# Performance work log

Measured on AMD Instinct MI355X. Metric: run time of the kernel, lower is better.

Reference implementation:

```python
import jax, jax.numpy as jnp
import numpy as np

B, N, D = 2, 2048, 2048
H, HKV, HD = 16, 4, 128  # n_heads, n_kv_heads, head_dim
G = H // HKV             # GQA group size


def setup_inputs() -> dict:
    key = jax.random.key(0)
    ks = jax.random.split(key, 5)
    x = jax.random.normal(ks[0], (B, N, D), jnp.float32)
    # rotary angles: standard 10000-base frequencies, half head_dim
    inv_freq = 1.0 / (10000.0 ** (jnp.arange(HD // 2, dtype=jnp.float32) / (HD // 2)))
    ang = jnp.arange(N, dtype=jnp.float32)[:, None] * inv_freq[None, :]  # [N, HD/2]
    cos = jnp.cos(ang)[None, :, None, :]  # [1, N, 1, HD/2]
    sin = jnp.sin(ang)[None, :, None, :]
    attn_mask = jnp.ones((B, N), jnp.float32)
    s = 0.02
    Wq = jax.random.normal(ks[1], (D, H * HD), jnp.float32) * s
    Wkv = jax.random.normal(ks[2], (D, 2 * HKV * HD), jnp.float32) * s
    Wo = jax.random.normal(ks[3], (H * HD, D), jnp.float32) * s
    bo = jnp.zeros((D,), jnp.float32)
    return {"x": x, "cos": cos, "sin": sin, "attn_mask": attn_mask,
            "Wq": Wq, "Wkv": Wkv, "Wo": Wo, "bo": bo}


def _rope(t, cos, sin):
    # t: [b, n, h, d]; rotate-half style split at d//2
    d2 = t.shape[-1] // 2
    t1, t2 = t[..., :d2], t[..., d2:]
    return jnp.concatenate([t1 * cos + t2 * sin, t2 * cos - t1 * sin], axis=-1)


def reference(x, cos, sin, attn_mask, Wq, Wkv, Wo, bo):
    b, n, _ = x.shape
    q = (x @ Wq).reshape(b, n, H, HD)
    kv = x @ Wkv
    k, v = jnp.split(kv, 2, axis=-1)
    k = k.reshape(b, n, HKV, HD)
    v = v.reshape(b, n, HKV, HD)
    q = _rope(q, cos, sin)
    k = _rope(k, cos, sin)
    # b n h d -> b h n d; group q heads: head H_idx maps to kv head H_idx % HKV
    # (einops '(r h)' repeat pattern => q reshaped as [b, G, HKV, n, d])
    q = q.transpose(0, 2, 1, 3).reshape(b, G, HKV, n, HD)
    k = k.transpose(0, 2, 1, 3)  # [b, HKV, n, d]
    v = v.transpose(0, 2, 1, 3)
    scale = HD ** -0.5
    attn = jnp.einsum('bghnd,bhmd->bghnm', q, k) * scale
    bias = (1.0 - attn_mask) * -1e9  # [b, n_keys]
    attn = attn + bias[:, None, None, None, :]
    attn = jax.nn.softmax(attn, axis=-1)
    out = jnp.einsum('bghnm,bhmd->bghnd', attn, v)
    # b (g h) n d -> b n (g h d)
    out = out.transpose(0, 3, 1, 2, 4).reshape(b, n, H * HD)
    return out @ Wo + bo
```

## Files before the change

### kernel.cpp

```cpp
#include <hip/hip_runtime.h>
#include <hip/hip_bf16.h>
#include <cstddef>

#define NB    2
#define NSEQ  2048
#define DMODEL 2048
#define NH    16
#define NKV   4
#define HDIM  128

typedef __attribute__((ext_vector_type(8))) short short8;
typedef __attribute__((ext_vector_type(4))) short short4v;
typedef __attribute__((ext_vector_type(4))) float floatx4;
typedef const __attribute__((address_space(1))) void* gptr_t;
typedef __attribute__((address_space(3))) void* lptr_t;

#if __has_builtin(__builtin_amdgcn_exp2f)
#define EXP2F(x) __builtin_amdgcn_exp2f(x)
#else
#define EXP2F(x) __expf((x) * 0.6931471805599453f)
#endif

__device__ inline unsigned short f2bf(float f) {
    unsigned int u = __float_as_uint(f);
    u += 0x7fffu + ((u >> 16) & 1u);
    return (unsigned short)(u >> 16);
}

__device__ inline floatx4 fzero4() {
    floatx4 v; v[0] = 0.f; v[1] = 0.f; v[2] = 0.f; v[3] = 0.f; return v;
}

__global__ void cast_f32_bf16(const float* __restrict__ in,
                              unsigned short* __restrict__ out, int n4) {
    int i = blockIdx.x * blockDim.x + threadIdx.x;
    if (i >= n4) return;
    float4 v = ((const float4*)in)[i];
    ushort4 o;
    o.x = f2bf(v.x); o.y = f2bf(v.y); o.z = f2bf(v.z); o.w = f2bf(v.w);
    ((ushort4*)out)[i] = o;
}

__global__ void transpose_cast(const float* __restrict__ W,
                               unsigned short* __restrict__ Wt, int K, int N) {
    __shared__ float tile[32][33];
    int tx = threadIdx.x, ty = threadIdx.y;
    int n0 = blockIdx.x * 32, k0 = blockIdx.y * 32;
#pragma unroll
    for (int i = 0; i < 4; i++)
        tile[ty + i * 8][tx] = W[(size_t)(k0 + ty + i * 8) * N + n0 + tx];
    __syncthreads();
#pragma unroll
    for (int i = 0; i < 4; i++)
        Wt[(size_t)(n0 + ty + i * 8) * K + k0 + tx] = f2bf(tile[tx][ty + i * 8]);
}

__global__ __launch_bounds__(256, 2) void gemm_bt(
    const unsigned short* __restrict__ A,
    const unsigned short* __restrict__ Bt,
    float* __restrict__ C,
    const float* __restrict__ bias,
    int M, int N, int K) {
    __shared__ __align__(16) unsigned short As[128 * 32];
    __shared__ __align__(16) unsigned short Bs[128 * 32];
    const int t = threadIdx.x;
    const int m0 = blockIdx.y * 128, n0 = blockIdx.x * 128;
    const int lane = t & 63, wave = t >> 6;
    const int ln = lane & 15, quad = lane >> 4;
    const int wm = (wave >> 1) * 64, wn = (wave & 1) * 64;
    floatx4 acc[4][4];
#pragma unroll
    for (int r = 0; r < 4; r++)
#pragma unroll
        for (int c = 0; c < 4; c++) acc[r][c] = fzero4();

    const int r0 = t >> 2, c0 = (t & 3) * 8;
    const int r1 = (t + 256) >> 2, c1 = ((t + 256) & 3) * 8;

    for (int kt = 0; kt < K; kt += 32) {
        const unsigned short* ga0 = A + (size_t)(m0 + r0) * K + kt + c0;
        const unsigned short* ga1 = A + (size_t)(m0 + r1) * K + kt + c1;
        const unsigned short* gb0 = Bt + (size_t)(n0 + r0) * K + kt + c0;
        const unsigned short* gb1 = Bt + (size_t)(n0 + r1) * K + kt + c1;
        __builtin_amdgcn_global_load_lds((gptr_t)ga0, (lptr_t)(As + t * 8), 16, 0, 0);
        __builtin_amdgcn_global_load_lds((gptr_t)ga1, (lptr_t)(As + (t + 256) * 8), 16, 0, 0);
        __builtin_amdgcn_global_load_lds((gptr_t)gb0, (lptr_t)(Bs + t * 8), 16, 0, 0);
        __builtin_amdgcn_global_load_lds((gptr_t)gb1, (lptr_t)(Bs + (t + 256) * 8), 16, 0, 0);
        __syncthreads();
        short8 af[4], bfr[4];
#pragma unroll
        for (int r = 0; r < 4; r++)
            af[r] = *(const short8*)(As + (wm + r * 16 + ln) * 32 + quad * 8);
#pragma unroll
        for (int c = 0; c < 4; c++)
            bfr[c] = *(const short8*)(Bs + (wn + c * 16 + ln) * 32 + quad * 8);
#pragma unroll
        for (int r = 0; r < 4; r++)
#pragma unroll
            for (int c = 0; c < 4; c++)
                acc[r][c] = __builtin_amdgcn_mfma_f32_16x16x32_bf16(af[r], bfr[c], acc[r][c], 0, 0, 0);
        __syncthreads();
    }
#pragma unroll
    for (int r = 0; r < 4; r++) {
        int mb = m0 + wm + r * 16 + quad * 4;
#pragma unroll
        for (int c = 0; c < 4; c++) {
            int col = n0 + wn + c * 16 + ln;
            float bv = bias ? bias[col] : 0.f;
#pragma unroll
            for (int g = 0; g < 4; g++)
                C[(size_t)(mb + g) * N + col] = acc[r][c][g] + bv;
        }
    }
}

__global__ void rope_q_k(const float* __restrict__ qkv, const float* __restrict__ cosb,
                         const float* __restrict__ sinb, unsigned short* __restrict__ Qb) {
    int idx = blockIdx.x * blockDim.x + threadIdx.x;
    int j = idx & 63;
    int h = (idx >> 6) & 15;
    int n = (idx >> 10) & 2047;
    int b = idx >> 21;
    const float scale = (float)(0.08838834764831845 * 1.4426950408889634);
    size_t row = (size_t)(b * NSEQ + n) * 3072;
    float t1 = qkv[row + h * 128 + j];
    float t2 = qkv[row + h * 128 + j + 64];
    float c = cosb[n * 64 + j], s = sinb[n * 64 + j];
    size_t orow = ((size_t)(b * NH + h) * NSEQ + n) * 128;
    Qb[orow + j]      = f2bf((t1 * c + t2 * s) * scale);
    Qb[orow + j + 64] = f2bf((t2 * c - t1 * s) * scale);
}

__global__ void rope_kv_k(const float* __restrict__ qkv, const float* __restrict__ cosb,
                          const float* __restrict__ sinb, unsigned short* __restrict__ Kb,
                          unsigned short* __restrict__ Vt) {
    int idx = blockIdx.x * blockDim.x + threadIdx.x;
    int j = idx & 63;
    int hk = (idx >> 6) & 3;
    int n = (idx >> 8) & 2047;
    int b = idx >> 19;
    size_t row = (size_t)(b * NSEQ + n) * 3072;
    float t1 = qkv[row + 2048 + hk * 128 + j];
    float t2 = qkv[row + 2048 + hk * 128 + j + 64];
    float c = cosb[n * 64 + j], s = sinb[n * 64 + j];
    size_t orow = ((size_t)(b * NKV + hk) * NSEQ + n) * 128;
    Kb[orow + j]      = f2bf(t1 * c + t2 * s);
    Kb[orow + j + 64] = f2bf(t2 * c - t1 * s);
    float v1 = qkv[row + 2560 + hk * 128 + j];
    float v2 = qkv[row + 2560 + hk * 128 + j + 64];
    int r = n & 63;
    int rp = ((r >> 5) << 5) | (((r >> 2) & 3) << 3) | (((r >> 4) & 1) << 2) | (r & 3);
    int np = (n & ~63) | rp;
    size_t vbase = (size_t)(b * NKV + hk) * 128 * NSEQ;
    Vt[vbase + (size_t)j * NSEQ + np]        = f2bf(v1);
    Vt[vbase + (size_t)(j + 64) * NSEQ + np] = f2bf(v2);
}

__global__ __launch_bounds__(256, 2) void attn_k(
    const unsigned short* __restrict__ Qb,
    const unsigned short* __restrict__ Kb,
    const unsigned short* __restrict__ Vt,
    const float* __restrict__ mask,
    unsigned short* __restrict__ Ab) {
    __shared__ __align__(16) unsigned short Ks[2 * 64 * 128];
    __shared__ __align__(16) unsigned short Vs[2 * 128 * 64];
    const int t = threadIdx.x, wave = t >> 6, lane = t & 63;
    const int ln = lane & 15, quad = lane >> 4;
    const int y = blockIdx.y, b = y >> 4, h = y & 15, kv = h & 3;
    const int q0 = blockIdx.x * 128;

    const unsigned short* Kbase = Kb + (size_t)(b * NKV + kv) * NSEQ * 128;
    const unsigned short* Vbase = Vt + (size_t)(b * NKV + kv) * 128 * NSEQ;
    const float* mbase = mask + b * NSEQ;

    const unsigned short* Qp =
        Qb + ((size_t)(b * NH + h) * NSEQ + q0 + wave * 32 + ln) * 128;
    short8 qf[2][4];
#pragma unroll
    for (int rt = 0; rt < 2; rt++)
#pragma unroll
        for (int kc = 0; kc < 4; kc++)
            qf[rt][kc] = *(const short8*)(Qp + rt * 16 * 128 + kc * 32 + quad * 8);

    floatx4 Oacc[2][8];
#pragma unroll
    for (int rt = 0; rt < 2; rt++)
#pragma unroll
        for (int d = 0; d < 8; d++) Oacc[rt][d] = fzero4();
    floatx4 Lacc[2];
    Lacc[0] = fzero4(); Lacc[1] = fzero4();

    short8 ones8;
#pragma unroll
    for (int i = 0; i < 8; i++) ones8[i] = (short)0x3F80;

    {
#pragma unroll
        for (int i = 0; i < 4; i++) {
            int c = i * 256 + t, r = c >> 4, c8 = c & 15;
            __builtin_amdgcn_global_load_lds(
                (gptr_t)(Kbase + (size_t)r * 128 + ((c8 ^ (r & 7)) * 8)),
                (lptr_t)(Ks + c * 8), 16, 0, 0);
        }
#pragma unroll
        for (int i = 0; i < 4; i++) {
            int c = i * 256 + t, dr = c >> 3, c8 = c & 7;
            __builtin_amdgcn_global_load_lds(
                (gptr_t)(Vbase + (size_t)dr * NSEQ + ((c8 ^ (dr & 7)) * 8)),
                (lptr_t)(Vs + c * 8), 16, 0, 0);
        }
    }
    __syncthreads();

    for (int it = 0; it < NSEQ / 64; ++it) {
        const int kt = it * 64, cb = it & 1;
        const int ktn = (kt + 64) & (NSEQ - 1);
        unsigned short* Kn = Ks + (cb ^ 1) * 8192;
        unsigned short* Vn = Vs + (cb ^ 1) * 8192;
#pragma unroll
        for (int i = 0; i < 4; i++) {
            int c = i * 256 + t, r = c >> 4, c8 = c & 15;
            __builtin_amdgcn_global_load_lds(
                (gptr_t)(Kbase + (size_t)(ktn + r) * 128 + ((c8 ^ (r & 7)) * 8)),
                (lptr_t)(Kn + c * 8), 16, 0, 0);
        }
#pragma unroll
        for (int i = 0; i < 4; i++) {
            int c = i * 256 + t, dr = c >> 3, c8 = c & 7;
            __builtin_amdgcn_global_load_lds(
                (gptr_t)(Vbase + (size_t)dr * NSEQ + ktn + ((c8 ^ (dr & 7)) * 8)),
                (lptr_t)(Vn + c * 8), 16, 0, 0);
        }

        floatx4 biasv[4];
#pragma unroll
        for (int nj = 0; nj < 4; nj++) {
            float4 mb = *(const float4*)(mbase + kt + nj * 16 + quad * 4);
            biasv[nj][0] = (1.f - mb.x) * -1.4426950408889634e9f;
            biasv[nj][1] = (1.f - mb.y) * -1.4426950408889634e9f;
            biasv[nj][2] = (1.f - mb.z) * -1.4426950408889634e9f;
            biasv[nj][3] = (1.f - mb.w) * -1.4426950408889634e9f;
        }

        const unsigned short* Kc = Ks + cb * 8192;
        const unsigned short* Vc = Vs + cb * 8192;

        floatx4 sacc[2][4];
#pragma unroll
        for (int rt = 0; rt < 2; rt++)
#pragma unroll
            for (int nj = 0; nj < 4; nj++) sacc[rt][nj] = fzero4();
#pragma unroll
        for (int kc = 0; kc < 4; kc++) {
            short8 kfv[4];
#pragma unroll
            for (int nj = 0; nj < 4; nj++)
                kfv[nj] = *(const short8*)(
                    Kc + (nj * 16 + ln) * 128 + (((kc * 4 + quad) ^ (ln & 7)) * 8));
#pragma unroll
            for (int rt = 0; rt < 2; rt++)
#pragma unroll
                for (int nj = 0; nj < 4; nj++)
                    sacc[rt][nj] = __builtin_amdgcn_mfma_f32_16x16x32_bf16(
                        kfv[nj], qf[rt][kc], sacc[rt][nj], 0, 0, 0);
        }

        short8 pf[2][2];
#pragma unroll
        for (int rt = 0; rt < 2; rt++)
#pragma unroll
            for (int p = 0; p < 2; p++)
#pragma unroll
                for (int e = 0; e < 2; e++) {
                    int nj = 2 * p + e;
#pragma unroll
                    for (int g = 0; g < 4; g++) {
                        float v = EXP2F(sacc[rt][nj][g] + biasv[nj][g]);
                        pf[rt][p][e * 4 + g] = (short)f2bf(v);
                    }
                }

#pragma unroll
        for (int rt = 0; rt < 2; rt++)
#pragma unroll
            for (int p = 0; p < 2; p++)
                Lacc[rt] = __builtin_amdgcn_mfma_f32_16x16x32_bf16(
                    ones8, pf[rt][p], Lacc[rt], 0, 0, 0);

#pragma unroll
        for (int dt = 0; dt < 8; dt++) {
            short8 vf[2];
#pragma unroll
            for (int p = 0; p < 2; p++)
                vf[p] = *(const short8*)(
                    Vc + (dt * 16 + ln) * 64 + (((p * 4 + quad) ^ (ln & 7)) * 8));
#pragma unroll
            for (int rt = 0; rt < 2; rt++) {
                floatx4 o = Oacc[rt][dt];
                o = __builtin_amdgcn_mfma_f32_16x16x32_bf16(vf[0], pf[rt][0], o, 0, 0, 0);
                o = __builtin_amdgcn_mfma_f32_16x16x32_bf16(vf[1], pf[rt][1], o, 0, 0, 0);
                Oacc[rt][dt] = o;
            }
        }
        __syncthreads();
    }

#pragma unroll
    for (int rt = 0; rt < 2; rt++) {
        float inv = 1.f / Lacc[rt][0];
        int row = q0 + wave * 32 + rt * 16 + ln;
        unsigned short* outp = Ab + (size_t)(b * NSEQ + row) * 2048 + h * 128;
#pragma unroll
        for (int dt = 0; dt < 8; dt++) {
            short4v o4;
#pragma unroll
            for (int g = 0; g < 4; g++) o4[g] = (short)f2bf(Oacc[rt][dt][g] * inv);
            *(short4v*)(outp + dt * 16 + quad * 4) = o4;
        }
    }
}

extern "C" void kernel_launch(void* const* d_in, const int* in_sizes, int n_in,
                              void* d_out, int out_size, void* d_ws, size_t ws_size,
                              hipStream_t stream) {
    const float* x    = (const float*)d_in[0];
    const float* cosb = (const float*)d_in[1];
    const float* sinb = (const float*)d_in[2];
    const float* mask = (const float*)d_in[3];
    const float* Wq   = (const float*)d_in[4];
    const float* Wkv  = (const float*)d_in[5];
    const float* Wo   = (const float*)d_in[6];
    const float* bo   = (const float*)d_in[7];
    float* out = (float*)d_out;

    char* ws = (char*)d_ws;
    unsigned short* xb  = (unsigned short*)ws; ws += (size_t)4096 * 2048 * 2;
    unsigned short* W1T = (unsigned short*)ws; ws += (size_t)3072 * 2048 * 2;
    unsigned short* WoT = (unsigned short*)ws; ws += (size_t)2048 * 2048 * 2;
    unsigned short* Qb  = (unsigned short*)ws; ws += (size_t)2 * 16 * 2048 * 128 * 2;
    unsigned short* Kb  = (unsigned short*)ws; ws += (size_t)2 * 4 * 2048 * 128 * 2;
    unsigned short* Vt  = (unsigned short*)ws; ws += (size_t)2 * 4 * 2048 * 128 * 2;
    float* qkv = (float*)ws;                   ws += (size_t)4096 * 3072 * 4;
    unsigned short* Ab = (unsigned short*)qkv;

    cast_f32_bf16<<<8192, 256, 0, stream>>>(x, xb, 2097152);
    dim3 tb(32, 8);
    transpose_cast<<<dim3(64, 64), tb, 0, stream>>>(Wq, W1T, 2048, 2048);
    transpose_cast<<<dim3(32, 64), tb, 0, stream>>>(Wkv, W1T + (size_t)2048 * 2048, 2048, 1024);
    transpose_cast<<<dim3(64, 64), tb, 0, stream>>>(Wo, WoT, 2048, 2048);
    gemm_bt<<<dim3(24, 32), 256, 0, stream>>>(xb, W1T, qkv, nullptr, 4096, 3072, 2048);
    rope_q_k<<<16384, 256, 0, stream>>>(qkv, cosb, sinb, Qb);
    rope_kv_k<<<4096, 256, 0, stream>>>(qkv, cosb, sinb, Kb, Vt);
    attn_k<<<dim3(16, 32), 256, 0, stream>>>(Qb, Kb, Vt, mask, Ab);
    gemm_bt<<<dim3(16, 32), 256, 0, stream>>>(Ab, WoT, out, bo, 4096, 2048, 2048);
}
```

Before: 351.0 us.

## Fuse RoPE and Q/K/V layout writes into the QKV GEMM epilogue

Replaces the generic QKV GEMM plus two RoPE kernels with one GEMM whose epilogue applies rotary embedding to Q and K. It writes bf16 Q/K straight to their head-major layouts and transposes V through shared memory into the permuted Vt layout. B columns are remapped so each wave holds both rotary halves (j and j+64) in registers. This drops the large fp32 qkv intermediate round-trip and two launches. In exchange it adds extra LDS for the V staging tile and scattered 2-byte stores in the Q/K epilogue.

New measurement: 320.4 us. 8.7% less time.

```diff
diff --git a/kernel.cpp b/kernel.cpp
--- a/kernel.cpp
+++ b/kernel.cpp
@@ -115,46 +115,117 @@
     }
 }
 
-__global__ void rope_q_k(const float* __restrict__ qkv, const float* __restrict__ cosb,
-                         const float* __restrict__ sinb, unsigned short* __restrict__ Qb) {
-    int idx = blockIdx.x * blockDim.x + threadIdx.x;
-    int j = idx & 63;
-    int h = (idx >> 6) & 15;
-    int n = (idx >> 10) & 2047;
-    int b = idx >> 21;
-    const float scale = (float)(0.08838834764831845 * 1.4426950408889634);
-    size_t row = (size_t)(b * NSEQ + n) * 3072;
-    float t1 = qkv[row + h * 128 + j];
-    float t2 = qkv[row + h * 128 + j + 64];
-    float c = cosb[n * 64 + j], s = sinb[n * 64 + j];
-    size_t orow = ((size_t)(b * NH + h) * NSEQ + n) * 128;
-    Qb[orow + j]      = f2bf((t1 * c + t2 * s) * scale);
-    Qb[orow + j + 64] = f2bf((t2 * c - t1 * s) * scale);
-}
-
-__global__ void rope_kv_k(const float* __restrict__ qkv, const float* __restrict__ cosb,
-                          const float* __restrict__ sinb, unsigned short* __restrict__ Kb,
-                          unsigned short* __restrict__ Vt) {
-    int idx = blockIdx.x * blockDim.x + threadIdx.x;
-    int j = idx & 63;
-    int hk = (idx >> 6) & 3;
-    int n = (idx >> 8) & 2047;
-    int b = idx >> 19;
-    size_t row = (size_t)(b * NSEQ + n) * 3072;
-    float t1 = qkv[row + 2048 + hk * 128 + j];
-    float t2 = qkv[row + 2048 + hk * 128 + j + 64];
-    float c = cosb[n * 64 + j], s = sinb[n * 64 + j];
-    size_t orow = ((size_t)(b * NKV + hk) * NSEQ + n) * 128;
-    Kb[orow + j]      = f2bf(t1 * c + t2 * s);
-    Kb[orow + j + 64] = f2bf(t2 * c - t1 * s);
-    float v1 = qkv[row + 2560 + hk * 128 + j];
-    float v2 = qkv[row + 2560 + hk * 128 + j + 64];
-    int r = n & 63;
-    int rp = ((r >> 5) << 5) | (((r >> 2) & 3) << 3) | (((r >> 4) & 1) << 2) | (r & 3);
-    int np = (n & ~63) | rp;
-    size_t vbase = (size_t)(b * NKV + hk) * 128 * NSEQ;
-    Vt[vbase + (size_t)j * NSEQ + np]        = f2bf(v1);
-    Vt[vbase + (size_t)(j + 64) * NSEQ + np] = f2bf(v2);
+__global__ __launch_bounds__(256, 2) void gemm_qkv_rope(
+    const unsigned short* __restrict__ A,
+    const unsigned short* __restrict__ Bt,
+    const float* __restrict__ cosb,
+    const float* __restrict__ sinb,
+    unsigned short* __restrict__ Qb,
+    unsigned short* __restrict__ Kb,
+    unsigned short* __restrict__ Vt) {
+    const int K = DMODEL;
+    __shared__ __align__(16) unsigned short As[128 * 32];
+    __shared__ __align__(16) unsigned short Bs[128 * 32];
+    __shared__ __align__(16) unsigned short Vx[128 * 136];
+    const int t = threadIdx.x;
+    const int m0 = blockIdx.y * 128, n0 = blockIdx.x * 128;
+    const int lane = t & 63, wave = t >> 6;
+    const int ln = lane & 15, quad = lane >> 4;
+    const int wm = (wave >> 1) * 64, bq = (wave & 1) * 32;
+    floatx4 acc[4][4];
+#pragma unroll
+    for (int r = 0; r < 4; r++)
+#pragma unroll
+        for (int c = 0; c < 4; c++) acc[r][c] = fzero4();
+
+    const int r0 = t >> 2, c0 = (t & 3) * 8;
+    const int r1 = (t + 256) >> 2, c1 = ((t + 256) & 3) * 8;
+
+    for (int kt = 0; kt < K; kt += 32) {
+        const unsigned short* ga0 = A + (size_t)(m0 + r0) * K + kt + c0;
+        const unsigned short* ga1 = A + (size_t)(m0 + r1) * K + kt + c1;
+        const unsigned short* gb0 = Bt + (size_t)(n0 + r0) * K + kt + c0;
+        const unsigned short* gb1 = Bt + (size_t)(n0 + r1) * K + kt + c1;
+        __builtin_amdgcn_global_load_lds((gptr_t)ga0, (lptr_t)(As + t * 8), 16, 0, 0);
+        __builtin_amdgcn_global_load_lds((gptr_t)ga1, (lptr_t)(As + (t + 256) * 8), 16, 0, 0);
+        __builtin_amdgcn_global_load_lds((gptr_t)gb0, (lptr_t)(Bs + t * 8), 16, 0, 0);
+        __builtin_amdgcn_global_load_lds((gptr_t)gb1, (lptr_t)(Bs + (t + 256) * 8), 16, 0, 0);
+        __syncthreads();
+        short8 af[4], bfr[4];
+#pragma unroll
+        for (int r = 0; r < 4; r++)
+            af[r] = *(const short8*)(As + (wm + r * 16 + ln) * 32 + quad * 8);
+#pragma unroll
+        for (int c = 0; c < 4; c++)
+            bfr[c] = *(const short8*)(
+                Bs + (bq + (c & 1) * 16 + (c >> 1) * 64 + ln) * 32 + quad * 8);
+#pragma unroll
+        for (int r = 0; r < 4; r++)
+#pragma unroll
+            for (int c = 0; c < 4; c++)
+                acc[r][c] = __builtin_amdgcn_mfma_f32_16x16x32_bf16(af[r], bfr[c], acc[r][c], 0, 0, 0);
+        __syncthreads();
+    }
+
+    if (n0 < 2048) {
+        const float qs = (float)(0.08838834764831845 * 1.4426950408889634);
+        int h = n0 >> 7;
+#pragma unroll
+        for (int r = 0; r < 4; r++)
+#pragma unroll
+            for (int c = 0; c < 2; c++)
+#pragma unroll
+                for (int g = 0; g < 4; g++) {
+                    int row = m0 + wm + r * 16 + quad * 4 + g;
+                    int b = row >> 11, n = row & 2047;
+                    int j = bq + c * 16 + ln;
+                    float cv = cosb[n * 64 + j], sv = sinb[n * 64 + j];
+                    float t1 = acc[r][c][g], t2 = acc[r][c + 2][g];
+                    unsigned short* qp = Qb + ((size_t)(b * NH + h) * NSEQ + n) * 128;
+                    qp[j]      = f2bf((t1 * cv + t2 * sv) * qs);
+                    qp[j + 64] = f2bf((t2 * cv - t1 * sv) * qs);
+                }
+    } else if (n0 < 2560) {
+        int hk = (n0 - 2048) >> 7;
+#pragma unroll
+        for (int r = 0; r < 4; r++)
+#pragma unroll
+            for (int c = 0; c < 2; c++)
+#pragma unroll
+                for (int g = 0; g < 4; g++) {
+                    int row = m0 + wm + r * 16 + quad * 4 + g;
+                    int b = row >> 11, n = row & 2047;
+                    int j = bq + c * 16 + ln;
+                    float cv = cosb[n * 64 + j], sv = sinb[n * 64 + j];
+                    float t1 = acc[r][c][g], t2 = acc[r][c + 2][g];
+                    unsigned short* kp = Kb + ((size_t)(b * NKV + hk) * NSEQ + n) * 128;
+                    kp[j]      = f2bf(t1 * cv + t2 * sv);
+                    kp[j + 64] = f2bf(t2 * cv - t1 * sv);
+                }
+    } else {
+        int hk = (n0 - 2560) >> 7;
+#pragma unroll
+        for (int r = 0; r < 4; r++)
+#pragma unroll
+            for (int c = 0; c < 4; c++) {
+                int d = bq + (c & 1) * 16 + (c >> 1) * 64 + ln;
+                int s = wm + (r >> 1) * 32 + quad * 8 + (r & 1) * 4;
+#pragma unroll
+                for (int g = 0; g < 4; g++)
+                    Vx[d * 136 + s + g] = f2bf(acc[r][c][g]);
+            }
+        __syncthreads();
+        int b = m0 >> 11, nloc = m0 & 2047;
+#pragma unroll
+        for (int pass = 0; pass < 2; pass++) {
+            int d = pass * 64 + (t >> 2), q4 = t & 3;
+            unsigned short* vp =
+                Vt + ((size_t)(b * NKV + hk) * 128 + d) * NSEQ + nloc + q4 * 32;
+#pragma unroll
+            for (int i = 0; i < 4; i++)
+                *(short8*)(vp + i * 8) = *(const short8*)(Vx + d * 136 + q4 * 32 + i * 8);
+        }
+    }
 }
 
 __global__ __launch_bounds__(256, 2) void attn_k(
@@ -341,17 +412,14 @@
     unsigned short* Qb  = (unsigned short*)ws; ws += (size_t)2 * 16 * 2048 * 128 * 2;
     unsigned short* Kb  = (unsigned short*)ws; ws += (size_t)2 * 4 * 2048 * 128 * 2;
     unsigned short* Vt  = (unsigned short*)ws; ws += (size_t)2 * 4 * 2048 * 128 * 2;
-    float* qkv = (float*)ws;                   ws += (size_t)4096 * 3072 * 4;
-    unsigned short* Ab = (unsigned short*)qkv;
+    unsigned short* Ab  = (unsigned short*)ws; ws += (size_t)2 * 2048 * 2048 * 2;
 
     cast_f32_bf16<<<8192, 256, 0, stream>>>(x, xb, 2097152);
     dim3 tb(32, 8);
     transpose_cast<<<dim3(64, 64), tb, 0, stream>>>(Wq, W1T, 2048, 2048);
     transpose_cast<<<dim3(32, 64), tb, 0, stream>>>(Wkv, W1T + (size_t)2048 * 2048, 2048, 1024);
     transpose_cast<<<dim3(64, 64), tb, 0, stream>>>(Wo, WoT, 2048, 2048);
-    gemm_bt<<<dim3(24, 32), 256, 0, stream>>>(xb, W1T, qkv, nullptr, 4096, 3072, 2048);
-    rope_q_k<<<16384, 256, 0, stream>>>(qkv, cosb, sinb, Qb);
-    rope_kv_k<<<4096, 256, 0, stream>>>(qkv, cosb, sinb, Kb, Vt);
+    gemm_qkv_rope<<<dim3(24, 32), 256, 0, stream>>>(xb, W1T, cosb, sinb, Qb, Kb, Vt);
     attn_k<<<dim3(16, 32), 256, 0, stream>>>(Qb, Kb, Vt, mask, Ab);
     gemm_bt<<<dim3(16, 32), 256, 0, stream>>>(Ab, WoT, out, bo, 4096, 2048, 2048);
 }
```
